# Optimization experiments

Measured on AMD Instinct MI355X. Metric: run time of the kernel, lower is better.

Reference implementation:

```python
import jax, jax.numpy as jnp
import numpy as np

DIAG = 4  # number of distinct power-of-2 diagonal bands; must divide H


def _diag_mask(H, L):
    # head h in group g = h // (H // DIAG) uses tril diagonal offset 2**g - 1.
    # True entries are MASKED (filled with -inf), except the last key column
    # which is always kept (cur_mask[:, -1] = 0 in the torch code).
    group = H // DIAG
    offs = 2 ** (jnp.arange(H) // group) - 1            # [H]
    rows = jnp.arange(L)[:, None]                        # [L,1] query index
    cols = jnp.arange(L)[None, :]                        # [1,L] key index
    mask = (cols <= rows + offs[:, None, None]) & (cols != L - 1)  # [H,L,L]
    return mask


def setup_inputs() -> dict:
    key = jax.random.key(0)
    kq, kk, kv = jax.random.split(key, 3)
    B, L, H, E = 4, 2048, 16, 64
    queries = jax.random.normal(kq, (B, L, H, E), dtype=jnp.float32)
    keys = jax.random.normal(kk, (B, L, H, E), dtype=jnp.float32)
    values = jax.random.normal(kv, (B, L, H, E), dtype=jnp.float32)
    return {"queries": queries, "keys": keys, "values": values}


def reference(queries, keys, values):
    B, L, H, E = queries.shape
    scale = 1.0 / np.sqrt(E).astype(np.float32)
    # [B,H,L,S]
    scores = jnp.einsum('blhe,bshe->bhls', queries, keys)
    mask = _diag_mask(H, L)                              # [H,L,L]
    scores = jnp.where(mask[None], -jnp.inf, scores)
    A = jax.nn.softmax(scale * scores, axis=-1)          # dropout inactive (eval)
    V = jnp.einsum('bhls,bshd->blhd', A, values)
    return V
```

## Files before the change

kernel.cpp:

```cpp
#include <hip/hip_runtime.h>
#include <stdint.h>

using f32x4  = __attribute__((ext_vector_type(4))) float;
using f32x16 = __attribute__((ext_vector_type(16))) float;
using s16x8  = __attribute__((ext_vector_type(8))) short;
using u16x4  = __attribute__((ext_vector_type(4))) unsigned short;
using u32x4  = __attribute__((ext_vector_type(4))) unsigned int;

typedef __attribute__((address_space(3))) unsigned int lds_u32;
typedef __attribute__((address_space(1))) unsigned int glb_u32;

__device__ __forceinline__ unsigned short f2bf(float f){
  union { float f; unsigned u; } x; x.f = f;
  return (unsigned short)((x.u + 0x7FFFu + ((x.u >> 16) & 1u)) >> 16);
}
__device__ __forceinline__ unsigned cvt_pk(float lo, float hi){
  unsigned r;
  asm("v_cvt_pk_bf16_f32 %0, %1, %2" : "=v"(r) : "v"(lo), "v"(hi));
  return r;
}
__device__ __forceinline__ void plswap(unsigned &a, unsigned &b){
  asm volatile("v_permlane32_swap_b32 %0, %1" : "+v"(a), "+v"(b));
}

#if __has_builtin(__builtin_amdgcn_exp2f)
#define EXP2F(x) __builtin_amdgcn_exp2f(x)
#else
#define EXP2F(x) exp2f(x)
#endif

#define MFMA16(A,B,C) __builtin_amdgcn_mfma_f32_16x16x32_bf16((A),(B),(C),0,0,0)
#define MFMA32(A,B,C) __builtin_amdgcn_mfma_f32_32x32x16_bf16((A),(B),(C),0,0,0)

constexpr int   L      = 2048;
constexpr int   H      = 16;
constexpr int   E      = 64;
constexpr int   HE     = 1024;
constexpr float SCALE  = 0.125f;
constexpr float QSCALE = 0.18033688011112042f;

__global__ __launch_bounds__(256)
void prep_kv(const float* __restrict__ Kg, const float* __restrict__ Vg,
             unsigned short* __restrict__ Ko, unsigned short* __restrict__ Vo){
  __shared__ __align__(16) unsigned short t8[4096];
  const int g0 = blockIdx.x;
  const int t  = threadIdx.x;
  if (g0 < 2048){
    const int gid = g0;
    const int jt = gid & 31, bh = gid >> 5;
    const int b = bh >> 4, h = bh & 15;
    const int key6 = t >> 2;
    const int p    = t & 3;
    const int kb = key6 >> 5, k31 = key6 & 31;
    const float* src = Kg + ((size_t)((b*2048 + jt*64 + key6)*16 + h) << 6) + p*16;
    const float4 v0 = *reinterpret_cast<const float4*>(src);
    const float4 v1 = *reinterpret_cast<const float4*>(src + 4);
    const float4 v2 = *reinterpret_cast<const float4*>(src + 8);
    const float4 v3 = *reinterpret_cast<const float4*>(src + 12);
    s16x8 f0, f1;
    f0[0]=(short)f2bf(v0.x); f0[1]=(short)f2bf(v0.y); f0[2]=(short)f2bf(v0.z); f0[3]=(short)f2bf(v0.w);
    f0[4]=(short)f2bf(v1.x); f0[5]=(short)f2bf(v1.y); f0[6]=(short)f2bf(v1.z); f0[7]=(short)f2bf(v1.w);
    f1[0]=(short)f2bf(v2.x); f1[1]=(short)f2bf(v2.y); f1[2]=(short)f2bf(v2.z); f1[3]=(short)f2bf(v2.w);
    f1[4]=(short)f2bf(v3.x); f1[5]=(short)f2bf(v3.y); f1[6]=(short)f2bf(v3.z); f1[7]=(short)f2bf(v3.w);
    const int slot0 = ((kb*4 + p)*2 + 0)*32 + k31;
    *reinterpret_cast<s16x8*>(&t8[slot0*8])      = f0;
    *reinterpret_cast<s16x8*>(&t8[(slot0+32)*8]) = f1;
    __syncthreads();
    unsigned short* dst = Ko + ((size_t)gid << 12) + t*16;
    *reinterpret_cast<s16x8*>(dst)     = *reinterpret_cast<const s16x8*>(&t8[t*16]);
    *reinterpret_cast<s16x8*>(dst + 8) = *reinterpret_cast<const s16x8*>(&t8[t*16 + 8]);
  } else {
    const int gid = g0 - 2048;
    const int jt = gid & 31, bh = gid >> 5;
    const int b = bh >> 4, h = bh & 15;
    const int key6 = t >> 2;
    const int p    = t & 3;
    const int kc = key6 >> 4, h2 = (key6 >> 3) & 1, kr = key6 & 7;
    const float* src = Vg + ((size_t)((b*2048 + jt*64 + key6)*16 + h) << 6) + p*16;
    float vv[16];
    #pragma unroll
    for (int q = 0; q < 4; ++q){
      const float4 v = *reinterpret_cast<const float4*>(src + q*4);
      vv[q*4+0]=v.x; vv[q*4+1]=v.y; vv[q*4+2]=v.z; vv[q*4+3]=v.w;
    }
    #pragma unroll
    for (int j = 0; j < 16; ++j){
      const int e  = p*16 + j;
      const int eb = e >> 5, e31 = e & 31;
      const int slot = ((eb*4 + kc)*2 + h2)*32 + e31;
      t8[slot*8 + kr] = f2bf(vv[j]);
    }
    __syncthreads();
    unsigned short* dst = Vo + ((size_t)gid << 12) + t*16;
    *reinterpret_cast<s16x8*>(dst)     = *reinterpret_cast<const s16x8*>(&t8[t*16]);
    *reinterpret_cast<s16x8*>(dst + 8) = *reinterpret_cast<const s16x8*>(&t8[t*16 + 8]);
  }
}

__global__ __launch_bounds__(512, 4)
void attn14(const float* __restrict__ Qg, const unsigned short* __restrict__ Kbg,
            const unsigned short* __restrict__ Vtg, float* __restrict__ Og)
{
  __shared__ __align__(16) unsigned short Kbuf[2][8192];
  __shared__ __align__(16) unsigned short Vbuf[2][8192];

  const int tid  = threadIdx.x;
  const int wave = tid >> 6;
  const int lane = tid & 63;
  const int c    = lane & 31;
  const int hi   = lane >> 5;

  const int gid = blockIdx.x;
  const int u   = gid >> 6;
  const int bh  = gid & 63;
  const int qb  = (u < 4) ? u : (11 - u);
  const int b = bh >> 4, h = bh & 15;
  const int off = (1 << (h >> 2)) - 1;

  const int    qrow0 = 256 * qb + wave * 32;
  const size_t fbase = (size_t)b * L * HE + (size_t)h * 64;
  const size_t tbase = (size_t)bh * 32;

  s16x8 qf[4];
  {
    const float* qp_ = Qg + fbase + (size_t)(qrow0 + c) * HE;
    #pragma unroll
    for (int ec = 0; ec < 4; ++ec){
      const float4 a  = *reinterpret_cast<const float4*>(qp_ + ec*16 + hi*8);
      const float4 b2 = *reinterpret_cast<const float4*>(qp_ + ec*16 + hi*8 + 4);
      s16x8 v;
      v[0]=(short)f2bf(a.x*QSCALE);  v[1]=(short)f2bf(a.y*QSCALE);
      v[2]=(short)f2bf(a.z*QSCALE);  v[3]=(short)f2bf(a.w*QSCALE);
      v[4]=(short)f2bf(b2.x*QSCALE); v[5]=(short)f2bf(b2.y*QSCALE);
      v[6]=(short)f2bf(b2.z*QSCALE); v[7]=(short)f2bf(b2.w*QSCALE);
      qf[ec] = v;
    }
  }

  s16x8 ones;
  #pragma unroll
  for (int j = 0; j < 8; ++j) ones[j] = (short)0x3F80;

  f32x16 acc0, acc1, accl;
  #pragma unroll
  for (int r = 0; r < 16; ++r){ acc0[r]=0.f; acc1[r]=0.f; accl[r]=0.f; }

  const int j0   = 2 * qb;
  const int qlim = qrow0 + c + off;

  auto STAGE = [&](int jt, int nb){
    const unsigned short* gk = Kbg + ((size_t)(tbase + 2*jt) << 12) + (size_t)(wave*1024 + lane*8);
    const unsigned short* gv = Vtg + ((size_t)(tbase + 2*jt) << 12) + (size_t)(wave*1024 + lane*8);
    __builtin_amdgcn_global_load_lds((const glb_u32*)gk,
        (lds_u32*)&Kbuf[nb][wave*1024], 16, 0, 0);
    __builtin_amdgcn_global_load_lds((const glb_u32*)(gk + 512),
        (lds_u32*)&Kbuf[nb][wave*1024 + 512], 16, 0, 0);
    __builtin_amdgcn_global_load_lds((const glb_u32*)gv,
        (lds_u32*)&Vbuf[nb][wave*1024], 16, 0, 0);
    __builtin_amdgcn_global_load_lds((const glb_u32*)(gv + 512),
        (lds_u32*)&Vbuf[nb][wave*1024 + 512], 16, 0, 0);
  };

  auto SUB = [&](int s0, bool last, const unsigned short* KB, const unsigned short* VB){
    if (!last && (s0 + 63 <= qrow0 + off)) return;

    f32x16 S0, S1;
    #pragma unroll
    for (int r = 0; r < 16; ++r){ S0[r]=0.f; S1[r]=0.f; }
    __builtin_amdgcn_s_setprio(1);
    #pragma unroll
    for (int ec = 0; ec < 4; ++ec){
      const s16x8 k0 = *reinterpret_cast<const s16x8*>(&KB[(((0*4+ec)*2+hi)*32 + c)*8]);
      const s16x8 k1 = *reinterpret_cast<const s16x8*>(&KB[(((1*4+ec)*2+hi)*32 + c)*8]);
      S0 = MFMA32(k0, qf[ec], S0);
      S1 = MFMA32(k1, qf[ec], S1);
    }
    __builtin_amdgcn_s_setprio(0);

    if (last || (s0 <= qrow0 + 31 + off)){
      #pragma unroll
      for (int r = 0; r < 16; ++r){
        const int kg0 = s0 + (r&3) + 8*(r>>2) + 4*hi;
        const int kg1 = kg0 + 32;
        if (!((kg0 > qlim) || (kg0 == L-1))) S0[r] = -1e30f;
        if (!((kg1 > qlim) || (kg1 == L-1))) S1[r] = -1e30f;
      }
    }

    #pragma unroll
    for (int r = 0; r < 16; ++r){
      S0[r] = EXP2F(S0[r]);
      S1[r] = EXP2F(S1[r]);
    }

    __builtin_amdgcn_s_setprio(1);
    #define PV_STEP(Pv, kh, kcg) { \
      unsigned a0 = cvt_pk(Pv[8*(kh)+0], Pv[8*(kh)+1]); \
      unsigned a1 = cvt_pk(Pv[8*(kh)+2], Pv[8*(kh)+3]); \
      unsigned b0 = cvt_pk(Pv[8*(kh)+4], Pv[8*(kh)+5]); \
      unsigned b1 = cvt_pk(Pv[8*(kh)+6], Pv[8*(kh)+7]); \
      plswap(a0, b0); plswap(a1, b1); \
      u32x4 afu; afu[0]=a0; afu[1]=a1; afu[2]=b0; afu[3]=b1; \
      const s16x8 af = __builtin_bit_cast(s16x8, afu); \
      const s16x8 vf0 = *reinterpret_cast<const s16x8*>(&VB[(((0*4+(kcg))*2+hi)*32 + c)*8]); \
      const s16x8 vf1 = *reinterpret_cast<const s16x8*>(&VB[(((1*4+(kcg))*2+hi)*32 + c)*8]); \
      acc0 = MFMA32(af, vf0, acc0); \
      acc1 = MFMA32(af, vf1, acc1); \
      accl = MFMA32(af, ones, accl); \
    }
    PV_STEP(S0, 0, 0)
    PV_STEP(S0, 1, 1)
    PV_STEP(S1, 0, 2)
    PV_STEP(S1, 1, 3)
    #undef PV_STEP
    __builtin_amdgcn_s_setprio(0);
  };

  auto COMP = [&](int jt, int nb){
    const int s0 = jt * 128;
    if ((jt < 15) && (s0 + 127 <= qrow0 + off)) return;
    SUB(s0,      false,        &Kbuf[nb][0],    &Vbuf[nb][0]);
    SUB(s0 + 64, (jt == 15),   &Kbuf[nb][4096], &Vbuf[nb][4096]);
  };

  #define WAITBAR4 asm volatile("s_waitcnt vmcnt(4)\n\ts_barrier" ::: "memory")
  #define WAITBAR0 asm volatile("s_waitcnt vmcnt(0)\n\ts_barrier" ::: "memory")
  #define BARRIER  __builtin_amdgcn_s_barrier()

  STAGE(j0, 0);
  if (j0 + 1 < 16) STAGE(j0 + 1, 1);

  for (int jt = j0; jt < 14; ++jt){
    WAITBAR4;
    COMP(jt, jt & 1);
    BARRIER;
    STAGE(jt + 2, jt & 1);
  }
  if (j0 < 15){
    WAITBAR4;
    COMP(14, 0);
  }
  WAITBAR0;
  COMP(15, 1);

  #undef WAITBAR4
  #undef WAITBAR0
  #undef BARRIER

  #pragma unroll
  for (int r = 0; r < 16; ++r){
    const int rowr = (r&3) + 8*(r>>2) + 4*hi;
    const float li = 1.0f / accl[r];
    float* op = Og + fbase + (size_t)(qrow0 + rowr) * HE;
    op[c]      = acc0[r] * li;
    op[32 + c] = acc1[r] * li;
  }
}

__global__ __launch_bounds__(512)
void attn_band(const float* __restrict__ Qg, const float* __restrict__ Kg,
               const float* __restrict__ Vg, float* __restrict__ Og)
{
  __shared__ __align__(16) unsigned short Ks[64*64];
  __shared__ __align__(16) unsigned short Vs[64*64];
  __shared__ __align__(16) unsigned short Ps[8][16*64];
  const int tid  = threadIdx.x;
  const int wave = tid >> 6;
  const int lane = tid & 63;
  const int lo16 = lane & 15;
  const int hi4  = lane >> 4;
  const int gid = blockIdx.x;
  const int qb  = gid & 15;
  const int bh  = gid >> 4;
  const int b   = bh >> 4;
  const int h   = bh & 15;
  const int off = (1 << (h >> 2)) - 1;
  const int    r0   = qb * 128;
  const size_t base = (size_t)b * L * HE + (size_t)h * 64;
  const int qrow0 = r0 + wave * 16;
  s16x8 qf[2];
  {
    const float* qp = Qg + base + (size_t)(qrow0 + lo16) * HE;
    #pragma unroll
    for (int ec = 0; ec < 2; ++ec){
      const int e0 = ec*32 + hi4*8;
      s16x8 v;
      #pragma unroll
      for (int j = 0; j < 8; ++j) v[j] = (short)f2bf(qp[e0 + j]);
      qf[ec] = v;
    }
  }
  f32x4 acc[4];
  #pragma unroll
  for (int et = 0; et < 4; ++et) acc[et] = f32x4{0.f,0.f,0.f,0.f};
  float m_run[4], l_run[4];
  #pragma unroll
  for (int i = 0; i < 4; ++i){ m_run[i] = -1e30f; l_run[i] = 0.f; }
  const int j0 = (r0 + off + 1) >> 6;
  for (int jt = j0; jt < 32; ++jt){
    const int s0 = jt * 64;
    __syncthreads();
    {
      const int f4    = tid & 15;
      const int rbase = tid >> 4;
      #pragma unroll
      for (int p = 0; p < 2; ++p){
        const int row = p*32 + rbase;
        const float4 vv = *reinterpret_cast<const float4*>(
            Kg + base + (size_t)(s0 + row) * HE + f4*4);
        u16x4 w; w[0]=f2bf(vv.x); w[1]=f2bf(vv.y); w[2]=f2bf(vv.z); w[3]=f2bf(vv.w);
        const int idx = row*64 + ((f4*4) ^ ((row & 7) << 3));
        *reinterpret_cast<u16x4*>(&Ks[idx]) = w;
      }
    }
    {
      const int kb = tid >> 5;
      const int e0 = (tid & 31) * 2;
      float2 cc[4];
      #pragma unroll
      for (int j = 0; j < 4; ++j)
        cc[j] = *reinterpret_cast<const float2*>(
            Vg + base + (size_t)(s0 + 4*kb + j) * HE + e0);
      #pragma unroll
      for (int i = 0; i < 2; ++i){
        const int e = e0 + i;
        u16x4 w;
        w[0] = f2bf(i ? cc[0].y : cc[0].x);
        w[1] = f2bf(i ? cc[1].y : cc[1].x);
        w[2] = f2bf(i ? cc[2].y : cc[2].x);
        w[3] = f2bf(i ? cc[3].y : cc[3].x);
        const int idx = e*64 + ((kb*4) ^ ((e & 7) << 3));
        *reinterpret_cast<u16x4*>(&Vs[idx]) = w;
      }
    }
    __syncthreads();
    if (jt < 31 && s0 + 63 <= qrow0 + off) continue;
    f32x4 S[4];
    #pragma unroll
    for (int kt = 0; kt < 4; ++kt){
      const int key = kt*16 + lo16;
      f32x4 z = {0.f,0.f,0.f,0.f};
      #pragma unroll
      for (int ec = 0; ec < 2; ++ec){
        const int e = ec*32 + hi4*8;
        const s16x8 kf = *reinterpret_cast<const s16x8*>(
            &Ks[key*64 + (e ^ ((key & 7) << 3))]);
        z = MFMA16(qf[ec], kf, z);
      }
      S[kt] = z;
    }
    #pragma unroll
    for (int kt = 0; kt < 4; ++kt){
      const int kg = s0 + kt*16 + lo16;
      #pragma unroll
      for (int i = 0; i < 4; ++i){
        const int qg2 = qrow0 + hi4*4 + i;
        const bool ok = (kg > qg2 + off) || (kg == L-1);
        S[kt][i] = ok ? S[kt][i]*SCALE : -1e30f;
      }
    }
    #pragma unroll
    for (int i = 0; i < 4; ++i){
      float t = fmaxf(fmaxf(S[0][i],S[1][i]), fmaxf(S[2][i],S[3][i]));
      t = fmaxf(t, __shfl_xor(t,1));
      t = fmaxf(t, __shfl_xor(t,2));
      t = fmaxf(t, __shfl_xor(t,4));
      t = fmaxf(t, __shfl_xor(t,8));
      const float mn = fmaxf(m_run[i], t);
      const float rs = __expf(m_run[i] - mn);
      m_run[i]  = mn;
      l_run[i] *= rs;
      acc[0][i] *= rs; acc[1][i] *= rs; acc[2][i] *= rs; acc[3][i] *= rs;
    }
    unsigned short* pwv = Ps[wave];
    float rsum[4] = {0.f,0.f,0.f,0.f};
    #pragma unroll
    for (int kt = 0; kt < 4; ++kt){
      #pragma unroll
      for (int i = 0; i < 4; ++i){
        const float p = __expf(S[kt][i] - m_run[i]);
        rsum[i] += p;
        const int qr  = hi4*4 + i;
        const int col = kt*16 + lo16;
        pwv[qr*64 + (col ^ ((qr & 7) << 3))] = f2bf(p);
      }
    }
    #pragma unroll
    for (int i = 0; i < 4; ++i){
      float t = rsum[i];
      t += __shfl_xor(t,1); t += __shfl_xor(t,2);
      t += __shfl_xor(t,4); t += __shfl_xor(t,8);
      l_run[i] += t;
    }
    #pragma unroll
    for (int kc = 0; kc < 2; ++kc){
      const int kk = kc*32 + hi4*8;
      const s16x8 pf = *reinterpret_cast<const s16x8*>(
          &pwv[lo16*64 + (kk ^ ((lo16 & 7) << 3))]);
      #pragma unroll
      for (int et = 0; et < 4; ++et){
        const int e = et*16 + lo16;
        const s16x8 vf = *reinterpret_cast<const s16x8*>(
            &Vs[e*64 + (kk ^ ((e & 7) << 3))]);
        acc[et] = MFMA16(pf, vf, acc[et]);
      }
    }
  }
  #pragma unroll
  for (int i = 0; i < 4; ++i){
    const float inv = 1.0f / l_run[i];
    const int   qg2 = qrow0 + hi4*4 + i;
    float* op = Og + base + (size_t)qg2 * HE;
    #pragma unroll
    for (int et = 0; et < 4; ++et)
      op[et*16 + lo16] = acc[et][i] * inv;
  }
}

extern "C" void kernel_launch(void* const* d_in, const int* in_sizes, int n_in,
                              void* d_out, int out_size, void* d_ws, size_t ws_size,
                              hipStream_t stream) {
  const float* Q = (const float*)d_in[0];
  const float* K = (const float*)d_in[1];
  const float* V = (const float*)d_in[2];
  float* O = (float*)d_out;

  const size_t kb_bytes = (size_t)64 * 32 * 4096 * 2;
  const size_t need     = kb_bytes * 2;
  if (ws_size >= need) {
    unsigned short* Kb = (unsigned short*)d_ws;
    unsigned short* Vt = (unsigned short*)((char*)d_ws + kb_bytes);
    prep_kv<<<dim3(4096), dim3(256), 0, stream>>>(K, V, Kb, Vt);
    attn14 <<<dim3(512),  dim3(512), 0, stream>>>(Q, Kb, Vt, O);
  } else {
    attn_band<<<dim3(1024), dim3(512), 0, stream>>>(Q, K, V, O);
  }
}
```

Measured before the change: 70.85 us.

## Replace ones-MFMA row sum with VALU reduction and batch QK MFMAs per tile

Drops the extra MFMA against a ones vector that computed the softmax denominator and instead sums the exponentiated scores with VALU adds plus one cross-half shuffle into a per-lane running scalar. The lane's sum is redistributed to output rows with a shuffle at the end. Both 64-key subtiles' QK MFMAs are now issued back to back before the mask/exp/PV phases, to give more independent matrix work in flight. Launch bounds drop from 4 to 3 waves per SIMD to allow more registers for the extra live score tiles, at the cost of occupancy.

```diff
diff --git a/kernel.cpp b/kernel.cpp
--- a/kernel.cpp
+++ b/kernel.cpp
@@ -97,8 +97,8 @@
   }
 }
 
-__global__ __launch_bounds__(512, 4)
-void attn14(const float* __restrict__ Qg, const unsigned short* __restrict__ Kbg,
+__global__ __launch_bounds__(512, 3)
+void attn16(const float* __restrict__ Qg, const unsigned short* __restrict__ Kbg,
             const unsigned short* __restrict__ Vtg, float* __restrict__ Og)
 {
   __shared__ __align__(16) unsigned short Kbuf[2][8192];
@@ -137,13 +137,10 @@
     }
   }
 
-  s16x8 ones;
+  f32x16 acc0, acc1;
   #pragma unroll
-  for (int j = 0; j < 8; ++j) ones[j] = (short)0x3F80;
-
-  f32x16 acc0, acc1, accl;
-  #pragma unroll
-  for (int r = 0; r < 16; ++r){ acc0[r]=0.f; acc1[r]=0.f; accl[r]=0.f; }
+  for (int r = 0; r < 16; ++r){ acc0[r]=0.f; acc1[r]=0.f; }
+  float l_run = 0.f;
 
   const int j0   = 2 * qb;
   const int qlim = qrow0 + c + off;
@@ -161,66 +158,98 @@
         (lds_u32*)&Vbuf[nb][wave*1024 + 512], 16, 0, 0);
   };
 
-  auto SUB = [&](int s0, bool last, const unsigned short* KB, const unsigned short* VB){
-    if (!last && (s0 + 63 <= qrow0 + off)) return;
-
-    f32x16 S0, S1;
-    #pragma unroll
-    for (int r = 0; r < 16; ++r){ S0[r]=0.f; S1[r]=0.f; }
-    __builtin_amdgcn_s_setprio(1);
-    #pragma unroll
-    for (int ec = 0; ec < 4; ++ec){
-      const s16x8 k0 = *reinterpret_cast<const s16x8*>(&KB[(((0*4+ec)*2+hi)*32 + c)*8]);
-      const s16x8 k1 = *reinterpret_cast<const s16x8*>(&KB[(((1*4+ec)*2+hi)*32 + c)*8]);
-      S0 = MFMA32(k0, qf[ec], S0);
-      S1 = MFMA32(k1, qf[ec], S1);
-    }
-    __builtin_amdgcn_s_setprio(0);
-
-    if (last || (s0 <= qrow0 + 31 + off)){
-      #pragma unroll
-      for (int r = 0; r < 16; ++r){
-        const int kg0 = s0 + (r&3) + 8*(r>>2) + 4*hi;
-        const int kg1 = kg0 + 32;
-        if (!((kg0 > qlim) || (kg0 == L-1))) S0[r] = -1e30f;
-        if (!((kg1 > qlim) || (kg1 == L-1))) S1[r] = -1e30f;
-      }
-    }
-
-    #pragma unroll
-    for (int r = 0; r < 16; ++r){
-      S0[r] = EXP2F(S0[r]);
-      S1[r] = EXP2F(S1[r]);
-    }
-
-    __builtin_amdgcn_s_setprio(1);
-    #define PV_STEP(Pv, kh, kcg) { \
-      unsigned a0 = cvt_pk(Pv[8*(kh)+0], Pv[8*(kh)+1]); \
-      unsigned a1 = cvt_pk(Pv[8*(kh)+2], Pv[8*(kh)+3]); \
-      unsigned b0 = cvt_pk(Pv[8*(kh)+4], Pv[8*(kh)+5]); \
-      unsigned b1 = cvt_pk(Pv[8*(kh)+6], Pv[8*(kh)+7]); \
-      plswap(a0, b0); plswap(a1, b1); \
-      u32x4 afu; afu[0]=a0; afu[1]=a1; afu[2]=b0; afu[3]=b1; \
-      const s16x8 af = __builtin_bit_cast(s16x8, afu); \
-      const s16x8 vf0 = *reinterpret_cast<const s16x8*>(&VB[(((0*4+(kcg))*2+hi)*32 + c)*8]); \
-      const s16x8 vf1 = *reinterpret_cast<const s16x8*>(&VB[(((1*4+(kcg))*2+hi)*32 + c)*8]); \
-      acc0 = MFMA32(af, vf0, acc0); \
-      acc1 = MFMA32(af, vf1, acc1); \
-      accl = MFMA32(af, ones, accl); \
-    }
-    PV_STEP(S0, 0, 0)
-    PV_STEP(S0, 1, 1)
-    PV_STEP(S1, 0, 2)
-    PV_STEP(S1, 1, 3)
-    #undef PV_STEP
-    __builtin_amdgcn_s_setprio(0);
-  };
-
   auto COMP = [&](int jt, int nb){
     const int s0 = jt * 128;
     if ((jt < 15) && (s0 + 127 <= qrow0 + off)) return;
-    SUB(s0,      false,        &Kbuf[nb][0],    &Vbuf[nb][0]);
-    SUB(s0 + 64, (jt == 15),   &Kbuf[nb][4096], &Vbuf[nb][4096]);
+    const unsigned short* KB = Kbuf[nb];
+    const unsigned short* VB = Vbuf[nb];
+    const bool liveA = !(s0 + 63 <= qrow0 + off);
+    const int  s1 = s0 + 64;
+    const bool last = (jt == 15);
+
+    f32x16 Sa0, Sa1, Sb0, Sb1;
+
+    __builtin_amdgcn_s_setprio(1);
+    if (liveA){
+      #pragma unroll
+      for (int r = 0; r < 16; ++r){ Sa0[r]=0.f; Sa1[r]=0.f; }
+      #pragma unroll
+      for (int ec = 0; ec < 4; ++ec){
+        const s16x8 k0 = *reinterpret_cast<const s16x8*>(&KB[(((0*4+ec)*2+hi)*32 + c)*8]);
+        const s16x8 k1 = *reinterpret_cast<const s16x8*>(&KB[(((1*4+ec)*2+hi)*32 + c)*8]);
+        Sa0 = MFMA32(k0, qf[ec], Sa0);
+        Sa1 = MFMA32(k1, qf[ec], Sa1);
+      }
+    }
+    {
+      #pragma unroll
+      for (int r = 0; r < 16; ++r){ Sb0[r]=0.f; Sb1[r]=0.f; }
+      #pragma unroll
+      for (int ec = 0; ec < 4; ++ec){
+        const s16x8 k0 = *reinterpret_cast<const s16x8*>(&KB[4096 + (((0*4+ec)*2+hi)*32 + c)*8]);
+        const s16x8 k1 = *reinterpret_cast<const s16x8*>(&KB[4096 + (((1*4+ec)*2+hi)*32 + c)*8]);
+        Sb0 = MFMA32(k0, qf[ec], Sb0);
+        Sb1 = MFMA32(k1, qf[ec], Sb1);
+      }
+    }
+    __builtin_amdgcn_s_setprio(0);
+
+    #define FINISH(S0v, S1v, sbase, isLast, vbOff) {                         \
+      if ((isLast) || ((sbase) <= qrow0 + 31 + off)){                        \
+        _Pragma("unroll")                                                    \
+        for (int r = 0; r < 16; ++r){                                        \
+          const int kg0 = (sbase) + (r&3) + 8*(r>>2) + 4*hi;                 \
+          const int kg1 = kg0 + 32;                                          \
+          if (!((kg0 > qlim) || (kg0 == L-1))) S0v[r] = -1e30f;              \
+          if (!((kg1 > qlim) || (kg1 == L-1))) S1v[r] = -1e30f;              \
+        }                                                                    \
+      }                                                                      \
+      _Pragma("unroll")                                                      \
+      for (int r = 0; r < 16; ++r){                                          \
+        S0v[r] = EXP2F(S0v[r]);                                              \
+        S1v[r] = EXP2F(S1v[r]);                                              \
+      }                                                                      \
+      {                                                                      \
+        float p0=0.f,p1=0.f,p2=0.f,p3=0.f;                                   \
+        _Pragma("unroll")                                                    \
+        for (int r = 0; r < 16; r += 4){                                     \
+          p0 += S0v[r]   + S1v[r];                                           \
+          p1 += S0v[r+1] + S1v[r+1];                                         \
+          p2 += S0v[r+2] + S1v[r+2];                                         \
+          p3 += S0v[r+3] + S1v[r+3];                                         \
+        }                                                                    \
+        float ps = (p0 + p1) + (p2 + p3);                                    \
+        ps += __shfl_xor(ps, 32);                                            \
+        l_run += ps;                                                         \
+      }                                                                      \
+      __builtin_amdgcn_s_setprio(1);                                         \
+      _Pragma("unroll")                                                      \
+      for (int kh = 0; kh < 2; ++kh){                                        \
+        _Pragma("unroll")                                                    \
+        for (int half = 0; half < 2; ++half){                                \
+          const f32x16& Pv = half ? S1v : S0v;                               \
+          const int kcg = half*2 + kh;                                       \
+          unsigned a0 = cvt_pk(Pv[8*kh+0], Pv[8*kh+1]);                      \
+          unsigned a1 = cvt_pk(Pv[8*kh+2], Pv[8*kh+3]);                      \
+          unsigned b0 = cvt_pk(Pv[8*kh+4], Pv[8*kh+5]);                      \
+          unsigned b1 = cvt_pk(Pv[8*kh+6], Pv[8*kh+7]);                      \
+          plswap(a0, b0); plswap(a1, b1);                                    \
+          u32x4 afu; afu[0]=a0; afu[1]=a1; afu[2]=b0; afu[3]=b1;             \
+          const s16x8 af = __builtin_bit_cast(s16x8, afu);                   \
+          const s16x8 vf0 = *reinterpret_cast<const s16x8*>(                 \
+              &VB[(vbOff) + (((0*4+kcg)*2+hi)*32 + c)*8]);                   \
+          const s16x8 vf1 = *reinterpret_cast<const s16x8*>(                 \
+              &VB[(vbOff) + (((1*4+kcg)*2+hi)*32 + c)*8]);                   \
+          acc0 = MFMA32(af, vf0, acc0);                                      \
+          acc1 = MFMA32(af, vf1, acc1);                                      \
+        }                                                                    \
+      }                                                                      \
+      __builtin_amdgcn_s_setprio(0);                                         \
+    }
+
+    if (liveA) FINISH(Sa0, Sa1, s0, false, 0)
+    FINISH(Sb0, Sb1, s1, last, 4096)
+    #undef FINISH
   };
 
   #define WAITBAR4 asm volatile("s_waitcnt vmcnt(4)\n\ts_barrier" ::: "memory")
@@ -247,10 +276,11 @@
   #undef WAITBAR0
   #undef BARRIER
 
+  const float inv = 1.0f / l_run;
   #pragma unroll
   for (int r = 0; r < 16; ++r){
     const int rowr = (r&3) + 8*(r>>2) + 4*hi;
-    const float li = 1.0f / accl[r];
+    const float li = __shfl(inv, rowr);
     float* op = Og + fbase + (size_t)(qrow0 + rowr) * HE;
     op[c]      = acc0[r] * li;
     op[32 + c] = acc1[r] * li;
@@ -431,7 +461,7 @@
     unsigned short* Kb = (unsigned short*)d_ws;
     unsigned short* Vt = (unsigned short*)((char*)d_ws + kb_bytes);
     prep_kv<<<dim3(4096), dim3(256), 0, stream>>>(K, V, Kb, Vt);
-    attn14 <<<dim3(512),  dim3(512), 0, stream>>>(Q, Kb, Vt, O);
+    attn16 <<<dim3(512),  dim3(512), 0, stream>>>(Q, Kb, Vt, O);
   } else {
     attn_band<<<dim3(1024), dim3(512), 0, stream>>>(Q, K, V, O);
   }
```

After: 79.80 us. +12.6%, slower.
